# Kernel optimization log

Hardware: AMD Instinct MI355X
Metric: run time of the kernel (lower is better)

Reference implementation:

```python
import jax, jax.numpy as jnp
import numpy as np

B, T, FB, C = 2, 256, 128, 128
H_T, H_F, BAND = 4, 4, 16
INNER = 4 * C


def setup_inputs() -> dict:
    key = jax.random.key(0)
    ks = jax.random.split(key, 8)
    g = lambda k, shp: jax.random.normal(k, shp, jnp.float32) * 0.02
    return {
        "x": jax.random.normal(ks[0], (B, T, FB, C), jnp.float32),
        # temporal pre-norm + MHA (in_proj [3C,C], out_proj [C,C])
        "ln_t_w": jnp.ones((C,), jnp.float32), "ln_t_b": jnp.zeros((C,), jnp.float32),
        "t_wi": g(ks[1], (3 * C, C)), "t_bi": jnp.zeros((3 * C,), jnp.float32),
        "t_wo": g(ks[2], (C, C)), "t_bo": jnp.zeros((C,), jnp.float32),
        # frequency pre-norm + MHA
        "ln_f_w": jnp.ones((C,), jnp.float32), "ln_f_b": jnp.zeros((C,), jnp.float32),
        "f_wi": g(ks[3], (3 * C, C)), "f_bi": jnp.zeros((3 * C,), jnp.float32),
        "f_wo": g(ks[4], (C, C)), "f_bo": jnp.zeros((C,), jnp.float32),
        # FFN pre-norm + two linears
        "ln_n_w": jnp.ones((C,), jnp.float32), "ln_n_b": jnp.zeros((C,), jnp.float32),
        "w1": g(ks[5], (INNER, C)), "b1": jnp.zeros((INNER,), jnp.float32),
        "w2": g(ks[6], (C, INNER)), "b2": jnp.zeros((C,), jnp.float32),
    }


def _ln(x, w, b, eps=1e-5):
    mu = x.mean(-1, keepdims=True)
    var = ((x - mu) ** 2).mean(-1, keepdims=True)
    return (x - mu) * jax.lax.rsqrt(var + eps) * w + b


def _mha(x, wi, bi, wo, bo, h, mask):
    """torch.nn.MultiheadAttention equivalent. x: [..., S, C], mask: additive [S, S]."""
    c = x.shape[-1]
    dh = c // h
    qkv = x @ wi.T + bi
    q, k, v = jnp.split(qkv, 3, axis=-1)
    split = lambda t: t.reshape(t.shape[:-1] + (h, dh)).swapaxes(-2, -3)  # [..., h, S, dh]
    q, k, v = split(q), split(k), split(v)
    scores = jnp.einsum('...hqd,...hkd->...hqk', q, k) * (1.0 / np.sqrt(dh)) + mask
    attn = jax.nn.softmax(scores, axis=-1)
    o = jnp.einsum('...hqk,...hkd->...hqd', attn, v)
    o = o.swapaxes(-2, -3).reshape(x.shape)
    return o @ wo.T + bo


def _causal_mask(n):
    i = jnp.arange(n)
    return jnp.where(i[:, None] >= i[None, :], 0.0, -jnp.inf).astype(jnp.float32)


def _band_mask(n, band):
    i = jnp.arange(n)
    return jnp.where(jnp.abs(i[:, None] - i[None, :]) <= band, 0.0, -jnp.inf).astype(jnp.float32)


def reference(x, ln_t_w, ln_t_b, t_wi, t_bi, t_wo, t_bo,
              ln_f_w, ln_f_b, f_wi, f_bi, f_wo, f_bo,
              ln_n_w, ln_n_b, w1, b1, w2, b2):
    cm = _causal_mask(x.shape[1])      # [T, T]
    bm = _band_mask(x.shape[2], BAND)  # [F, F]
    # temporal causal MHSA per frequency bin (pre-norm residual)
    xt = _ln(x, ln_t_w, ln_t_b).transpose(0, 2, 1, 3)  # [B, F, T, C]
    x = x + _mha(xt, t_wi, t_bi, t_wo, t_bo, H_T, cm).transpose(0, 2, 1, 3)
    # banded local MHSA over frequency per time step
    xf = _ln(x, ln_f_w, ln_f_b)  # [B, T, F, C]
    x = x + _mha(xf, f_wi, f_bi, f_wo, f_bo, H_F, bm)
    # FFN (Linear -> exact GELU -> Linear)
    xn = _ln(x, ln_n_w, ln_n_b)
    h = jax.nn.gelu(xn @ w1.T + b1, approximate=False)
    x = x + (h @ w2.T + b2)
    return x
```

## Files before the change

kernel.cpp:

```cpp
#include <hip/hip_runtime.h>
#include <math.h>

typedef __bf16 bf16;
typedef __bf16 bf16x8 __attribute__((ext_vector_type(8)));
typedef __bf16 bf16x4 __attribute__((ext_vector_type(4)));
typedef __bf16 bf16x2 __attribute__((ext_vector_type(2)));
typedef float f32x4 __attribute__((ext_vector_type(4)));
typedef float f32x2 __attribute__((ext_vector_type(2)));
typedef float f32x16 __attribute__((ext_vector_type(16)));
typedef unsigned int u32;
typedef unsigned int u32x4 __attribute__((ext_vector_type(4)));

#define AS1 __attribute__((address_space(1)))
#define AS3 __attribute__((address_space(3)))

static __device__ __forceinline__ f32x4 mfma16(bf16x8 a, bf16x8 b, f32x4 c) {
    return __builtin_amdgcn_mfma_f32_16x16x32_bf16(a, b, c, 0, 0, 0);
}
static __device__ __forceinline__ f32x16 mfma32(bf16x8 a, bf16x8 b, f32x16 c) {
    return __builtin_amdgcn_mfma_f32_32x32x16_bf16(a, b, c, 0, 0, 0);
}
static __device__ __forceinline__ u32 pk2(float a, float b) {
    bf16x2 v; v[0] = (bf16)a; v[1] = (bf16)b;
    return __builtin_bit_cast(u32, v);
}
static __device__ __forceinline__ float gelu_f(float x) {
    float u = 0.7978845608f * x * __builtin_fmaf(0.044715f, x * x, 1.0f);
    float e = __expf(2.0f * u);
    return x - x * __builtin_amdgcn_rcpf(e + 1.0f);
}

__global__ __launch_bounds__(256) void cvt_w6(
    const float* __restrict__ s0, const float* __restrict__ s1,
    const float* __restrict__ s2, const float* __restrict__ s3,
    const float* __restrict__ s4, const float* __restrict__ s5,
    bf16* __restrict__ dst)
{
    int i = (blockIdx.x * 256 + threadIdx.x) * 4;
    const float* src; int off;
    if      (i <  49152) { src = s0; off = 0; }
    else if (i <  65536) { src = s1; off = 49152; }
    else if (i < 114688) { src = s2; off = 65536; }
    else if (i < 131072) { src = s3; off = 114688; }
    else if (i < 196608) { src = s4; off = 131072; }
    else                 { src = s5; off = 196608; }
    f32x4 v = *(const f32x4*)&src[i - off];
    bf16x4 b;
    b[0] = (bf16)v[0]; b[1] = (bf16)v[1]; b[2] = (bf16)v[2]; b[3] = (bf16)v[3];
    *(bf16x4*)&dst[i] = b;
}

template<int OUT_BF16, int RES, int RESBF, int GELU_, int LNF, int LNA, int KT, int NT>
__global__ __launch_bounds__(256) void gemm_rw(
    const bf16* __restrict__ A, const bf16* __restrict__ W,
    const float* __restrict__ bias, const void* __restrict__ res,
    void* __restrict__ outp, bf16* __restrict__ xnout,
    const float* __restrict__ lnw, const float* __restrict__ lnb,
    const float* __restrict__ xf, const float* __restrict__ lnaw,
    const float* __restrict__ lnab)
{
    constexpr int N = NT * 128;
    __shared__ __align__(16) bf16 Bs[128 * 64];
    const int tid  = threadIdx.x;
    const int lane = tid & 63;
    const int w    = tid >> 6;
    const int li = lane & 15, g = lane >> 4;
    const int m0 = blockIdx.x * 64;
    const int arow = m0 + w * 16 + li;
    const bf16* ap = A + (size_t)arow * KT;

    bf16x8 afrag[4];
    if constexpr (LNA) {
        int b = arow >> 15, f = (arow >> 8) & 127, t = arow & 255;
        const float* xp = xf + (((size_t)b * 256 + t) * 128 + f) * 128;
        f32x4 cv[8];
        #pragma unroll
        for (int cc = 0; cc < 4; ++cc) {
            cv[2 * cc]     = *(const f32x4*)&xp[cc * 32 + g * 8];
            cv[2 * cc + 1] = *(const f32x4*)&xp[cc * 32 + g * 8 + 4];
        }
        float sm = 0.f, sq = 0.f;
        #pragma unroll
        for (int i = 0; i < 8; ++i)
            #pragma unroll
            for (int j = 0; j < 4; ++j) { float v = cv[i][j]; sm += v; sq += v * v; }
        sm += __shfl_xor(sm, 16); sm += __shfl_xor(sm, 32);
        sq += __shfl_xor(sq, 16); sq += __shfl_xor(sq, 32);
        float mu = sm * 0.0078125f;
        float rs = rsqrtf(sq * 0.0078125f - mu * mu + 1e-5f);
        #pragma unroll
        for (int cc = 0; cc < 4; ++cc) {
            f32x4 w0 = *(const f32x4*)&lnaw[cc * 32 + g * 8];
            f32x4 w1 = *(const f32x4*)&lnaw[cc * 32 + g * 8 + 4];
            f32x4 b0 = *(const f32x4*)&lnab[cc * 32 + g * 8];
            f32x4 b1 = *(const f32x4*)&lnab[cc * 32 + g * 8 + 4];
            #pragma unroll
            for (int j = 0; j < 4; ++j) {
                afrag[cc][j]     = (bf16)((cv[2 * cc][j]     - mu) * rs * w0[j] + b0[j]);
                afrag[cc][4 + j] = (bf16)((cv[2 * cc + 1][j] - mu) * rs * w1[j] + b1[j]);
            }
        }
    } else if constexpr (KT == 128) {
        #pragma unroll
        for (int cc = 0; cc < 4; ++cc)
            afrag[cc] = *(const bf16x8*)&ap[cc * 32 + g * 8];
    }

    #pragma unroll
    for (int t = 0; t < NT; ++t) {
        const int n0 = t * 128;
        f32x4 acc[8] = {};

        #pragma unroll
        for (int k0 = 0; k0 < KT; k0 += 64) {
            #pragma unroll
            for (int it = 0; it < 4; ++it) {
                int idx = it * 256 + tid;
                int brow = idx >> 3, bch = idx & 7;
                const bf16* gp = W + (size_t)(n0 + brow) * KT + k0 + ((bch ^ (brow & 7)) * 8);
                __builtin_amdgcn_global_load_lds((AS1 void*)gp, (AS3 void*)(Bs + idx * 8), 16, 0, 0);
            }
            bf16x8 av0, av1;
            if constexpr (KT != 128) {
                av0 = *(const bf16x8*)&ap[k0 + g * 8];
                av1 = *(const bf16x8*)&ap[k0 + 32 + g * 8];
            }
            __syncthreads();
            #pragma unroll
            for (int kk = 0; kk < 2; ++kk) {
                bf16x8 av;
                if constexpr (KT == 128) av = afrag[(k0 >> 5) + kk];
                else                     av = kk ? av1 : av0;
                #pragma unroll
                for (int j = 0; j < 8; ++j) {
                    int brow = j * 16 + li;
                    int bch = (kk * 4 + g) ^ (li & 7);
                    bf16x8 bv = *(const bf16x8*)&Bs[brow * 64 + bch * 8];
                    acc[j] = mfma16(av, bv, acc[j]);
                }
            }
            __syncthreads();
        }

        float bcol[8], lw[8], lb[8];
        #pragma unroll
        for (int j = 0; j < 8; ++j) {
            bcol[j] = bias[n0 + j * 16 + li];
            if constexpr (LNF) { lw[j] = lnw[j * 16 + li]; lb[j] = lnb[j * 16 + li]; }
        }

        const int row0 = m0 + w * 16 + g * 4;
        #pragma unroll
        for (int r = 0; r < 4; ++r) {
            int row = row0 + r;
            float vals[8];
            #pragma unroll
            for (int j = 0; j < 8; ++j) {
                float v = acc[j][r] + bcol[j];
                if constexpr (RES) {
                    size_t off = (size_t)row * N + n0 + j * 16 + li;
                    if constexpr (RESBF) v += (float)((const bf16*)res)[off];
                    else                 v += ((const float*)res)[off];
                }
                if constexpr (GELU_) v = gelu_f(v);
                vals[j] = v;
            }
            #pragma unroll
            for (int j = 0; j < 8; ++j) {
                size_t off = (size_t)row * N + n0 + j * 16 + li;
                if constexpr (OUT_BF16) ((bf16*)outp)[off] = (bf16)vals[j];
                else                    ((float*)outp)[off] = vals[j];
            }
            if constexpr (LNF) {
                float sm = 0.f, sq = 0.f;
                #pragma unroll
                for (int j = 0; j < 8; ++j) { sm += vals[j]; sq += vals[j] * vals[j]; }
                #pragma unroll
                for (int off = 1; off < 16; off <<= 1) {
                    sm += __shfl_xor(sm, off);
                    sq += __shfl_xor(sq, off);
                }
                float mu  = sm * 0.0078125f;
                float var = sq * 0.0078125f - mu * mu;
                float rs  = rsqrtf(var + 1e-5f);
                #pragma unroll
                for (int j = 0; j < 8; ++j)
                    xnout[(size_t)row * 128 + j * 16 + li] =
                        (bf16)((vals[j] - mu) * rs * lw[j] + lb[j]);
            }
        }
    }
}

template<int MODE>
__global__ __launch_bounds__(256) void attn_k(
    const bf16* __restrict__ qkv, bf16* __restrict__ o)
{
    constexpr int S = (MODE == 0) ? 256 : 128;
    const int lane = threadIdx.x & 63;
    const int w = threadIdx.x >> 6;
    const int hi = lane >> 5;
    const int q31 = lane & 31;
    const int s = blockIdx.x;
    const int h = blockIdx.y;
    const int qb = (MODE == 0) ? ((int)blockIdx.z * 128 + w * 32) : (w * 32);
    const int q = qb + q31;

    const size_t base = (size_t)s * S * 384;
    const bf16* qp = qkv + base + h * 32;
    const bf16* kp = qp + 128;
    const bf16* vp = qp + 256 + q31;

    bf16x8 qf0 = *(const bf16x8*)&qp[(size_t)q * 384 + hi * 8];
    bf16x8 qf1 = *(const bf16x8*)&qp[(size_t)q * 384 + 16 + hi * 8];

    f32x16 O = {};
    float m = -1e30f, l = 0.f;

    int klo, khi;
    if constexpr (MODE == 0) { klo = 0; khi = qb + 32; }
    else {
        klo = (qb > 16 ? (qb - 16) : 0) & ~31;
        khi = (qb + 48 < S) ? (qb + 48) : S;
    }

    const float sc = 0.17677669529663687f;

    for (int k0 = klo; k0 < khi; k0 += 32) {
        bf16x8 kf0 = *(const bf16x8*)&kp[(size_t)(k0 + q31) * 384 + hi * 8];
        bf16x8 kf1 = *(const bf16x8*)&kp[(size_t)(k0 + q31) * 384 + 16 + hi * 8];
        bf16x8 vf1, vf2;
        #pragma unroll
        for (int e = 0; e < 8; ++e) {
            vf1[e] = vp[(size_t)(k0 + hi * 8 + e) * 384];
            vf2[e] = vp[(size_t)(k0 + 16 + hi * 8 + e) * 384];
        }

        f32x16 st = {};
        st = mfma32(kf0, qf0, st);
        st = mfma32(kf1, qf1, st);

        float mx = -3.0e38f;
        #pragma unroll
        for (int r = 0; r < 16; ++r) {
            int krow = k0 + (r & 3) + 8 * (r >> 2) + 4 * hi;
            bool ok;
            if constexpr (MODE == 0) ok = (krow <= q);
            else { int d = krow - q; ok = (d <= 16 && d >= -16); }
            float v = ok ? st[r] * sc : -3.0e38f;
            st[r] = v;
            mx = fmaxf(mx, v);
        }
        mx = fmaxf(mx, __shfl_xor(mx, 32));
        float mn = fmaxf(m, mx);
        float resc = __expf(m - mn);
        m = mn;
        float ps = 0.f;
        #pragma unroll
        for (int r = 0; r < 16; ++r) {
            float p = __expf(st[r] - mn);
            st[r] = p;
            ps += p;
        }
        ps += __shfl_xor(ps, 32);
        l = l * resc + ps;
        #pragma unroll
        for (int r = 0; r < 16; ++r) O[r] *= resc;

        u32 c01 = pk2(st[0], st[1]),   c23 = pk2(st[2], st[3]);
        u32 c45 = pk2(st[4], st[5]),   c67 = pk2(st[6], st[7]);
        u32 c89 = pk2(st[8], st[9]),   cAB = pk2(st[10], st[11]);
        u32 cCD = pk2(st[12], st[13]), cEF = pk2(st[14], st[15]);
        u32 x01 = __shfl_xor((int)c01, 32), x23 = __shfl_xor((int)c23, 32);
        u32 x45 = __shfl_xor((int)c45, 32), x67 = __shfl_xor((int)c67, 32);
        u32 x89 = __shfl_xor((int)c89, 32), xAB = __shfl_xor((int)cAB, 32);
        u32 xCD = __shfl_xor((int)cCD, 32), xEF = __shfl_xor((int)cEF, 32);
        u32x4 b1w = hi ? u32x4{x45, x67, c45, c67} : u32x4{c01, c23, x01, x23};
        u32x4 b2w = hi ? u32x4{xCD, xEF, cCD, cEF} : u32x4{c89, cAB, x89, xAB};
        bf16x8 B1 = __builtin_bit_cast(bf16x8, b1w);
        bf16x8 B2 = __builtin_bit_cast(bf16x8, b2w);

        O = mfma32(vf1, B1, O);
        O = mfma32(vf2, B2, O);
    }

    float inv = 1.f / l;
    size_t orow;
    if constexpr (MODE == 0) {
        int b = s >> 7, f = s & 127;
        orow = ((size_t)(b * 256 + q)) * 128 + f;
    } else {
        orow = (size_t)s * 128 + q;
    }
    bf16* op = o + orow * 128 + h * 32;
    #pragma unroll
    for (int mb = 0; mb < 4; ++mb) {
        bf16x4 ov;
        #pragma unroll
        for (int j = 0; j < 4; ++j) ov[j] = (bf16)(O[mb * 4 + j] * inv);
        *(bf16x4*)&op[mb * 8 + hi * 4] = ov;
    }
}

extern "C" void kernel_launch(void* const* d_in, const int* in_sizes, int n_in,
                              void* d_out, int out_size, void* d_ws, size_t ws_size,
                              hipStream_t stream) {
    const float* x      = (const float*)d_in[0];
    const float* ln_t_w = (const float*)d_in[1];
    const float* ln_t_b = (const float*)d_in[2];
    const float* t_wi   = (const float*)d_in[3];
    const float* t_bi   = (const float*)d_in[4];
    const float* t_wo   = (const float*)d_in[5];
    const float* t_bo   = (const float*)d_in[6];
    const float* ln_f_w = (const float*)d_in[7];
    const float* ln_f_b = (const float*)d_in[8];
    const float* f_wi   = (const float*)d_in[9];
    const float* f_bi   = (const float*)d_in[10];
    const float* f_wo   = (const float*)d_in[11];
    const float* f_bo   = (const float*)d_in[12];
    const float* ln_n_w = (const float*)d_in[13];
    const float* ln_n_b = (const float*)d_in[14];
    const float* w1     = (const float*)d_in[15];
    const float* b1     = (const float*)d_in[16];
    const float* w2     = (const float*)d_in[17];
    const float* b2     = (const float*)d_in[18];

    char* ws = (char*)d_ws;
    bf16* wbf  = (bf16*)ws;
    bf16* xn   = (bf16*)(ws + 524288);
    bf16* qkvh = (bf16*)(ws + 524288 + 16777216);
    bf16* obf  = (bf16*)(ws + 524288 + 16777216 + 67108864);
    bf16* xcA  = (bf16*)(ws + 524288 + 16777216 + 67108864 + 16777216);
    bf16* xcB  = (bf16*)(ws + 524288 + 16777216 + 67108864 + 2 * 16777216);
    float* out = (float*)d_out;

    const bf16* twi_b = wbf + 0;
    const bf16* two_b = wbf + 49152;
    const bf16* fwi_b = wbf + 65536;
    const bf16* fwo_b = wbf + 114688;
    const bf16* w1_b  = wbf + 131072;
    const bf16* w2_b  = wbf + 196608;

    cvt_w6<<<256, 256, 0, stream>>>(t_wi, t_wo, f_wi, f_wo, w1, w2, wbf);

    gemm_rw<1, 0, 0, 0, 0, 1, 128, 3><<<1024, 256, 0, stream>>>(
        nullptr, twi_b, t_bi, nullptr, qkvh, nullptr, nullptr, nullptr,
        x, ln_t_w, ln_t_b);
    attn_k<0><<<dim3(256, 4, 2), 256, 0, stream>>>(qkvh, obf);
    gemm_rw<1, 1, 0, 0, 1, 0, 128, 1><<<1024, 256, 0, stream>>>(
        obf, two_b, t_bo, x, xcA, xn, ln_f_w, ln_f_b, nullptr, nullptr, nullptr);

    gemm_rw<1, 0, 0, 0, 0, 0, 128, 3><<<1024, 256, 0, stream>>>(
        xn, fwi_b, f_bi, nullptr, qkvh, nullptr, nullptr, nullptr,
        nullptr, nullptr, nullptr);
    attn_k<1><<<dim3(512, 4), 256, 0, stream>>>(qkvh, obf);
    gemm_rw<1, 1, 1, 0, 1, 0, 128, 1><<<1024, 256, 0, stream>>>(
        obf, fwo_b, f_bo, xcA, xcB, xn, ln_n_w, ln_n_b, nullptr, nullptr, nullptr);

    gemm_rw<1, 0, 0, 1, 0, 0, 128, 4><<<1024, 256, 0, stream>>>(
        xn, w1_b, b1, nullptr, qkvh, nullptr, nullptr, nullptr,
        nullptr, nullptr, nullptr);
    gemm_rw<0, 1, 1, 0, 0, 0, 512, 1><<<1024, 256, 0, stream>>>(
        qkvh, w2_b, b2, xcB, out, nullptr, nullptr, nullptr,
        nullptr, nullptr, nullptr);

    (void)in_sizes; (void)n_in; (void)out_size; (void)ws_size;
}
```

Measured before the change: 169.7 us.

## Fuse attention output projection, residual and LayerNorm into attention kernels

The attention kernels now handle all 4 heads for a 32-query tile in one block, with one head per wave. The normalized outputs are staged in LDS, and the block runs the Wo projection with MFMA, adds bias and the residual, and computes the following LayerNorm through a cross-wave LDS reduction. This drops two separate out-projection GEMM launches and the global round trip of the attention output buffer. In exchange, each block reads Wo straight from global memory without LDS reuse, and the causal temporal grid now puts imbalanced work into separate 32-query blocks.

```diff
diff --git a/kernel.cpp b/kernel.cpp
--- a/kernel.cpp
+++ b/kernel.cpp
@@ -50,12 +50,11 @@
     *(bf16x4*)&dst[i] = b;
 }
 
-template<int OUT_BF16, int RES, int RESBF, int GELU_, int LNF, int LNA, int KT, int NT>
+template<int OUT_BF16, int RES, int RESBF, int GELU_, int LNA, int KT, int NT>
 __global__ __launch_bounds__(256) void gemm_rw(
     const bf16* __restrict__ A, const bf16* __restrict__ W,
     const float* __restrict__ bias, const void* __restrict__ res,
-    void* __restrict__ outp, bf16* __restrict__ xnout,
-    const float* __restrict__ lnw, const float* __restrict__ lnb,
+    void* __restrict__ outp,
     const float* __restrict__ xf, const float* __restrict__ lnaw,
     const float* __restrict__ lnab)
 {
@@ -142,72 +141,50 @@
             __syncthreads();
         }
 
-        float bcol[8], lw[8], lb[8];
-        #pragma unroll
-        for (int j = 0; j < 8; ++j) {
-            bcol[j] = bias[n0 + j * 16 + li];
-            if constexpr (LNF) { lw[j] = lnw[j * 16 + li]; lb[j] = lnb[j * 16 + li]; }
-        }
+        float bcol[8];
+        #pragma unroll
+        for (int j = 0; j < 8; ++j) bcol[j] = bias[n0 + j * 16 + li];
 
         const int row0 = m0 + w * 16 + g * 4;
         #pragma unroll
         for (int r = 0; r < 4; ++r) {
             int row = row0 + r;
-            float vals[8];
             #pragma unroll
             for (int j = 0; j < 8; ++j) {
+                size_t off = (size_t)row * N + n0 + j * 16 + li;
                 float v = acc[j][r] + bcol[j];
                 if constexpr (RES) {
-                    size_t off = (size_t)row * N + n0 + j * 16 + li;
                     if constexpr (RESBF) v += (float)((const bf16*)res)[off];
                     else                 v += ((const float*)res)[off];
                 }
                 if constexpr (GELU_) v = gelu_f(v);
-                vals[j] = v;
-            }
-            #pragma unroll
-            for (int j = 0; j < 8; ++j) {
-                size_t off = (size_t)row * N + n0 + j * 16 + li;
-                if constexpr (OUT_BF16) ((bf16*)outp)[off] = (bf16)vals[j];
-                else                    ((float*)outp)[off] = vals[j];
-            }
-            if constexpr (LNF) {
-                float sm = 0.f, sq = 0.f;
-                #pragma unroll
-                for (int j = 0; j < 8; ++j) { sm += vals[j]; sq += vals[j] * vals[j]; }
-                #pragma unroll
-                for (int off = 1; off < 16; off <<= 1) {
-                    sm += __shfl_xor(sm, off);
-                    sq += __shfl_xor(sq, off);
-                }
-                float mu  = sm * 0.0078125f;
-                float var = sq * 0.0078125f - mu * mu;
-                float rs  = rsqrtf(var + 1e-5f);
-                #pragma unroll
-                for (int j = 0; j < 8; ++j)
-                    xnout[(size_t)row * 128 + j * 16 + li] =
-                        (bf16)((vals[j] - mu) * rs * lw[j] + lb[j]);
-            }
-        }
-    }
-}
-
-template<int MODE>
-__global__ __launch_bounds__(256) void attn_k(
-    const bf16* __restrict__ qkv, bf16* __restrict__ o)
+                if constexpr (OUT_BF16) ((bf16*)outp)[off] = (bf16)v;
+                else                    ((float*)outp)[off] = v;
+            }
+        }
+    }
+}
+
+template<int MODE, int RESBF>
+__global__ __launch_bounds__(256) void attn_fused(
+    const bf16* __restrict__ qkv, const bf16* __restrict__ Wo,
+    const float* __restrict__ bo, const void* __restrict__ res,
+    bf16* __restrict__ xc, bf16* __restrict__ xn,
+    const float* __restrict__ lnw, const float* __restrict__ lnb)
 {
     constexpr int S = (MODE == 0) ? 256 : 128;
+    __shared__ __align__(16) bf16 o_lds[32 * 136];
+    __shared__ float red[32][4][2];
     const int lane = threadIdx.x & 63;
     const int w = threadIdx.x >> 6;
     const int hi = lane >> 5;
     const int q31 = lane & 31;
     const int s = blockIdx.x;
-    const int h = blockIdx.y;
-    const int qb = (MODE == 0) ? ((int)blockIdx.z * 128 + w * 32) : (w * 32);
+    const int qb = blockIdx.y * 32;
     const int q = qb + q31;
 
     const size_t base = (size_t)s * S * 384;
-    const bf16* qp = qkv + base + h * 32;
+    const bf16* qp = qkv + base + w * 32;
     const bf16* kp = qp + 128;
     const bf16* vp = qp + 256 + q31;
 
@@ -285,20 +262,94 @@
     }
 
     float inv = 1.f / l;
-    size_t orow;
-    if constexpr (MODE == 0) {
-        int b = s >> 7, f = s & 127;
-        orow = ((size_t)(b * 256 + q)) * 128 + f;
-    } else {
-        orow = (size_t)s * 128 + q;
-    }
-    bf16* op = o + orow * 128 + h * 32;
     #pragma unroll
     for (int mb = 0; mb < 4; ++mb) {
         bf16x4 ov;
         #pragma unroll
         for (int j = 0; j < 4; ++j) ov[j] = (bf16)(O[mb * 4 + j] * inv);
-        *(bf16x4*)&op[mb * 8 + hi * 4] = ov;
+        *(bf16x4*)&o_lds[q31 * 136 + w * 32 + mb * 8 + hi * 4] = ov;
+    }
+    __syncthreads();
+
+    const int li = lane & 15, g = lane >> 4;
+    bf16x8 af[2][4];
+    #pragma unroll
+    for (int mi = 0; mi < 2; ++mi)
+        #pragma unroll
+        for (int kk = 0; kk < 4; ++kk)
+            af[mi][kk] = *(const bf16x8*)&o_lds[(mi * 16 + li) * 136 + kk * 32 + g * 8];
+
+    f32x4 acc[2][2] = {};
+    #pragma unroll
+    for (int ni = 0; ni < 2; ++ni) {
+        #pragma unroll
+        for (int kk = 0; kk < 4; ++kk) {
+            bf16x8 bv = *(const bf16x8*)&Wo[(size_t)(w * 32 + ni * 16 + li) * 128 + kk * 32 + g * 8];
+            acc[0][ni] = mfma16(af[0][kk], bv, acc[0][ni]);
+            acc[1][ni] = mfma16(af[1][kk], bv, acc[1][ni]);
+        }
+    }
+
+    int b0_ = 0, f0_ = 0;
+    if constexpr (MODE == 0) { b0_ = s >> 7; f0_ = s & 127; }
+    float vals[2][2][4];
+    size_t groff[2][4];
+    #pragma unroll
+    for (int mi = 0; mi < 2; ++mi) {
+        #pragma unroll
+        for (int r = 0; r < 4; ++r) {
+            int mrow = qb + mi * 16 + g * 4 + r;
+            size_t orow;
+            if constexpr (MODE == 0) orow = ((size_t)(b0_ * 256 + mrow)) * 128 + f0_;
+            else                     orow = (size_t)s * 128 + mrow;
+            groff[mi][r] = orow * 128;
+            #pragma unroll
+            for (int ni = 0; ni < 2; ++ni) {
+                int col = w * 32 + ni * 16 + li;
+                float v = acc[mi][ni][r] + bo[col];
+                if constexpr (RESBF) v += (float)((const bf16*)res)[groff[mi][r] + col];
+                else                 v += ((const float*)res)[groff[mi][r] + col];
+                vals[mi][ni][r] = v;
+            }
+        }
+    }
+    #pragma unroll
+    for (int mi = 0; mi < 2; ++mi) {
+        #pragma unroll
+        for (int r = 0; r < 4; ++r) {
+            float sm = vals[mi][0][r] + vals[mi][1][r];
+            float sq = vals[mi][0][r] * vals[mi][0][r] + vals[mi][1][r] * vals[mi][1][r];
+            #pragma unroll
+            for (int off = 1; off < 16; off <<= 1) {
+                sm += __shfl_xor(sm, off);
+                sq += __shfl_xor(sq, off);
+            }
+            if (li == 0) {
+                red[mi * 16 + g * 4 + r][w][0] = sm;
+                red[mi * 16 + g * 4 + r][w][1] = sq;
+            }
+        }
+    }
+    __syncthreads();
+    #pragma unroll
+    for (int mi = 0; mi < 2; ++mi) {
+        #pragma unroll
+        for (int r = 0; r < 4; ++r) {
+            int mrow = mi * 16 + g * 4 + r;
+            f32x4 p0 = *(const f32x4*)&red[mrow][0][0];
+            f32x4 p1 = *(const f32x4*)&red[mrow][2][0];
+            float smt = p0[0] + p0[2] + p1[0] + p1[2];
+            float sqt = p0[1] + p0[3] + p1[1] + p1[3];
+            float mu = smt * 0.0078125f;
+            float rs = rsqrtf(sqt * 0.0078125f - mu * mu + 1e-5f);
+            #pragma unroll
+            for (int ni = 0; ni < 2; ++ni) {
+                int col = w * 32 + ni * 16 + li;
+                float v = vals[mi][ni][r];
+                xc[groff[mi][r] + col] = (bf16)v;
+                xn[groff[mi][r] + col] = (bf16)((v - mu) * rs * lnw[col] + lnb[col]);
+            }
+        }
     }
 }
 
@@ -329,7 +380,6 @@
     bf16* wbf  = (bf16*)ws;
     bf16* xn   = (bf16*)(ws + 524288);
     bf16* qkvh = (bf16*)(ws + 524288 + 16777216);
-    bf16* obf  = (bf16*)(ws + 524288 + 16777216 + 67108864);
     bf16* xcA  = (bf16*)(ws + 524288 + 16777216 + 67108864 + 16777216);
     bf16* xcB  = (bf16*)(ws + 524288 + 16777216 + 67108864 + 2 * 16777216);
     float* out = (float*)d_out;
@@ -343,26 +393,20 @@
 
     cvt_w6<<<256, 256, 0, stream>>>(t_wi, t_wo, f_wi, f_wo, w1, w2, wbf);
 
-    gemm_rw<1, 0, 0, 0, 0, 1, 128, 3><<<1024, 256, 0, stream>>>(
-        nullptr, twi_b, t_bi, nullptr, qkvh, nullptr, nullptr, nullptr,
-        x, ln_t_w, ln_t_b);
-    attn_k<0><<<dim3(256, 4, 2), 256, 0, stream>>>(qkvh, obf);
-    gemm_rw<1, 1, 0, 0, 1, 0, 128, 1><<<1024, 256, 0, stream>>>(
-        obf, two_b, t_bo, x, xcA, xn, ln_f_w, ln_f_b, nullptr, nullptr, nullptr);
-
-    gemm_rw<1, 0, 0, 0, 0, 0, 128, 3><<<1024, 256, 0, stream>>>(
-        xn, fwi_b, f_bi, nullptr, qkvh, nullptr, nullptr, nullptr,
-        nullptr, nullptr, nullptr);
-    attn_k<1><<<dim3(512, 4), 256, 0, stream>>>(qkvh, obf);
-    gemm_rw<1, 1, 1, 0, 1, 0, 128, 1><<<1024, 256, 0, stream>>>(
-        obf, fwo_b, f_bo, xcA, xcB, xn, ln_n_w, ln_n_b, nullptr, nullptr, nullptr);
-
-    gemm_rw<1, 0, 0, 1, 0, 0, 128, 4><<<1024, 256, 0, stream>>>(
-        xn, w1_b, b1, nullptr, qkvh, nullptr, nullptr, nullptr,
-        nullptr, nullptr, nullptr);
-    gemm_rw<0, 1, 1, 0, 0, 0, 512, 1><<<1024, 256, 0, stream>>>(
-        qkvh, w2_b, b2, xcB, out, nullptr, nullptr, nullptr,
-        nullptr, nullptr, nullptr);
+    gemm_rw<1, 0, 0, 0, 1, 128, 3><<<1024, 256, 0, stream>>>(
+        nullptr, twi_b, t_bi, nullptr, qkvh, x, ln_t_w, ln_t_b);
+    attn_fused<0, 0><<<dim3(256, 8), 256, 0, stream>>>(
+        qkvh, two_b, t_bo, x, xcA, xn, ln_f_w, ln_f_b);
+
+    gemm_rw<1, 0, 0, 0, 0, 128, 3><<<1024, 256, 0, stream>>>(
+        xn, fwi_b, f_bi, nullptr, qkvh, nullptr, nullptr, nullptr);
+    attn_fused<1, 1><<<dim3(512, 4), 256, 0, stream>>>(
+        qkvh, fwo_b, f_bo, xcA, xcB, xn, ln_n_w, ln_n_b);
+
+    gemm_rw<1, 0, 0, 1, 0, 128, 4><<<1024, 256, 0, stream>>>(
+        xn, w1_b, b1, nullptr, qkvh, nullptr, nullptr, nullptr);
+    gemm_rw<0, 1, 1, 0, 0, 512, 1><<<1024, 256, 0, stream>>>(
+        qkvh, w2_b, b2, xcB, out, nullptr, nullptr, nullptr);
 
     (void)in_sizes; (void)n_in; (void)out_size; (void)ws_size;
 }
```

New measurement: 165.9 us. -2.2%, faster.
